# Optimization experiments

Hardware: AMD Instinct MI355X
Metric: run time of the kernel (lower is better)

## Reference

```python
import jax, jax.numpy as jnp
import numpy as np

L = 64       # num_steps
NHID = 256   # nhid
N = 64       # cache_N
TOPK = 8     # cache_k


def setup_inputs() -> dict:
    key = jax.random.key(0)
    k1, k2, k3 = jax.random.split(key, 3)
    query = jax.random.normal(k1, (1, L, 32, NHID), dtype=jnp.float32)
    keys = jax.random.normal(k2, (N, 32, L * NHID), dtype=jnp.float32)       # stacked key_i buffers
    values = jax.random.normal(k3, (N, L, 32, 4 * NHID), dtype=jnp.float32)  # stacked value_i buffers, (nlayers+1)*nhid=1024
    return {"query": query, "keys": keys, "values": values}


def reference(query, keys, values):
    # query: (query_len=1, L, bsz, nhid) -> transpose(1,2) -> (1, bsz, L, nhid)
    q = jnp.swapaxes(query, 1, 2)
    qlen, bsz = q.shape[0], q.shape[1]
    q = q.reshape(qlen, bsz, -1)                 # no_summary: (1, bsz, dk)
    keys_t = jnp.swapaxes(keys, 0, 1)            # (bsz, N, dk)
    _vals = jnp.einsum('klbh->bklh', values)     # (bsz, N, L, h); computed in original, unused in max_pooling branch
    # max_pooling branch
    q2 = q.reshape(-1, L, NHID)                  # (bsz, L, nhid)
    pk = keys_t.reshape(-1, N, L, NHID)          # (bsz, N, L, nhid)
    att = jnp.einsum('bih,bnjh->bijn', q2, pk)   # (bsz, L, L, N)
    att = att.reshape(-1, L * L, 1, N).max(axis=1)  # (bsz, 1, N) max-pool over all step pairs
    att = att.reshape(-1, 1, N)
    _, topk_idx = jax.lax.top_k(att, TOPK)       # (bsz, 1, topk)
    topk_idx = jnp.squeeze(topk_idx, axis=1).T   # (topk, bsz)
    return att, topk_idx
```

## Files before the change

kernel.cpp:

```cpp
#include <hip/hip_runtime.h>
#include <hip/hip_bf16.h>
#include <math.h>

namespace {

constexpr int L   = 64;
constexpr int NH  = 256;
constexpr int NC  = 64;
constexpr int BSZ = 32;

typedef float f32x16 __attribute__((ext_vector_type(16)));
typedef short bf16x8 __attribute__((ext_vector_type(8)));

__device__ inline void split8(const float4 x0, const float4 x1,
                              bf16x8& hi, bf16x8& lo) {
  float f[8];
  *(float4*)(f)     = x0;
  *(float4*)(f + 4) = x1;
#pragma unroll
  for (int q = 0; q < 8; ++q) {
    const __hip_bfloat16 h = __float2bfloat16(f[q]);
    unsigned short hu;
    __builtin_memcpy(&hu, &h, 2);
    const float hf = __builtin_bit_cast(float, (unsigned)hu << 16);
    const __hip_bfloat16 l = __float2bfloat16(f[q] - hf);
    unsigned short lu;
    __builtin_memcpy(&lu, &l, 2);
    hi[q] = (short)hu;
    lo[q] = (short)lu;
  }
}

__global__ __launch_bounds__(256, 2) void attmax_mfma(
    const float* __restrict__ query,
    const float* __restrict__ keys,
    float* __restrict__ out)
{
  __shared__ __align__(16) short Qhi[2 * 16 * 64 * 8];
  __shared__ __align__(16) short Qlo[2 * 16 * 64 * 8];

  const unsigned X = blockIdx.x;
  const int b = ((X >> 7) << 3) | (X & 7);
  const int g = (X >> 3) & 15;

  const int tid  = threadIdx.x;
  const int w    = tid >> 6;
  const int lane = tid & 63;
  const int r    = lane & 31;
  const int h    = lane >> 5;

  for (int s = tid; s < 2048; s += 256) {
    const int it = s >> 10;
    const int kc = (s >> 6) & 15;
    const int sl = s & 63;
    const int row = it * 32 + (sl & 31);
    const int kof = kc * 16 + (sl >> 5) * 8;
    const float* src = query + ((size_t)row * BSZ + b) * NH + kof;
    bf16x8 hi, lo;
    split8(*(const float4*)src, *(const float4*)(src + 4), hi, lo);
    *(bf16x8*)&Qhi[s * 8] = hi;
    *(bf16x8*)&Qlo[s * 8] = lo;
  }
  __syncthreads();

  const int n = g * 4 + w;
  const float* kb = keys + ((size_t)n * BSZ + b) * (size_t)(L * NH);
  const float* kp = kb + (size_t)r * NH + h * 8;

  f32x16 acc[2][2];
#pragma unroll
  for (int i = 0; i < 2; ++i)
#pragma unroll
    for (int j = 0; j < 2; ++j)
#pragma unroll
      for (int e = 0; e < 16; ++e) acc[i][j][e] = 0.f;

  float4 bufA[4], bufB[4];

#define LOAD_K(buf, kc)                                                  \
  do {                                                                   \
    const float* p0 = kp + (kc) * 16;                                    \
    (buf)[0] = *(const float4*)(p0);                                     \
    (buf)[1] = *(const float4*)(p0 + 4);                                 \
    const float* p1 = p0 + 32 * NH;                                      \
    (buf)[2] = *(const float4*)(p1);                                     \
    (buf)[3] = *(const float4*)(p1 + 4);                                 \
  } while (0)

#define COMPUTE(buf, kc)                                                 \
  do {                                                                   \
    bf16x8 bh0, bl0, bh1, bl1;                                           \
    split8((buf)[0], (buf)[1], bh0, bl0);                                \
    split8((buf)[2], (buf)[3], bh1, bl1);                                \
    bf16x8 ah[2], al[2];                                                 \
    _Pragma("unroll")                                                    \
    for (int it = 0; it < 2; ++it) {                                     \
      const int slot = ((it * 16 + (kc)) * 64 + lane) * 8;               \
      ah[it] = *(const bf16x8*)&Qhi[slot];                               \
      al[it] = *(const bf16x8*)&Qlo[slot];                               \
    }                                                                    \
    _Pragma("unroll")                                                    \
    for (int it = 0; it < 2; ++it) {                                     \
      acc[it][0] = __builtin_amdgcn_mfma_f32_32x32x16_bf16(al[it], bh0, acc[it][0], 0, 0, 0); \
      acc[it][0] = __builtin_amdgcn_mfma_f32_32x32x16_bf16(ah[it], bl0, acc[it][0], 0, 0, 0); \
      acc[it][0] = __builtin_amdgcn_mfma_f32_32x32x16_bf16(ah[it], bh0, acc[it][0], 0, 0, 0); \
      acc[it][1] = __builtin_amdgcn_mfma_f32_32x32x16_bf16(al[it], bh1, acc[it][1], 0, 0, 0); \
      acc[it][1] = __builtin_amdgcn_mfma_f32_32x32x16_bf16(ah[it], bl1, acc[it][1], 0, 0, 0); \
      acc[it][1] = __builtin_amdgcn_mfma_f32_32x32x16_bf16(ah[it], bh1, acc[it][1], 0, 0, 0); \
    }                                                                    \
  } while (0)

  LOAD_K(bufA, 0);
#pragma unroll
  for (int kc = 0; kc < 16; kc += 2) {
    if (kc + 1 < 16) LOAD_K(bufB, kc + 1);
    COMPUTE(bufA, kc);
    if (kc + 2 < 16) LOAD_K(bufA, kc + 2);
    COMPUTE(bufB, kc + 1);
  }
#undef LOAD_K
#undef COMPUTE

  float m = -INFINITY;
#pragma unroll
  for (int i = 0; i < 2; ++i)
#pragma unroll
    for (int j = 0; j < 2; ++j)
#pragma unroll
      for (int e = 0; e < 16; ++e) m = fmaxf(m, acc[i][j][e]);

#pragma unroll
  for (int off = 1; off < 64; off <<= 1)
    m = fmaxf(m, __shfl_xor(m, off, 64));

  if (lane == 0) out[(size_t)b * NC + n] = m;
}

__global__ __launch_bounds__(64) void topk_kernel(float* __restrict__ out) {
  const int b = blockIdx.x;
  const int l = threadIdx.x;
  float v = out[b * NC + l];
#pragma unroll
  for (int k = 0; k < 8; ++k) {
    float bv = v;
    int bi = l;
#pragma unroll
    for (int off = 1; off < 64; off <<= 1) {
      const float ov = __shfl_xor(bv, off, 64);
      const int oi = __shfl_xor(bi, off, 64);
      if (ov > bv || (ov == bv && oi < bi)) { bv = ov; bi = oi; }
    }
    if (l == 0) out[BSZ * NC + k * BSZ + b] = (float)bi;
    if (l == bi) v = -INFINITY;
  }
}

}

extern "C" void kernel_launch(void* const* d_in, const int* in_sizes, int n_in,
                              void* d_out, int out_size, void* d_ws, size_t ws_size,
                              hipStream_t stream) {
  const float* query = (const float*)d_in[0];
  const float* keys  = (const float*)d_in[1];
  float* out = (float*)d_out;

  attmax_mfma<<<dim3(512), dim3(256), 0, stream>>>(query, keys, out);
  topk_kernel<<<dim3(BSZ), dim3(64), 0, stream>>>(out);
}
```

Measured before the change: 38.99 us.

## Precompute split query once per batch and double waves per key

The bf16 hi/lo split of the query moves into a separate kernel that writes it to workspace once per batch element. The main kernel then copies that data into LDS with global_load_lds. The main kernel now runs 512 threads per block, with two waves per key vector, each handling half of the key rows. This cuts per-wave register use and raises parallelism for the memory-bound key stream. The two waves' partial maxima are combined through shared memory. The cost is one extra kernel launch, a workspace round trip, and a 64KB LDS footprint per block. That footprint may limit residency below the requested 4 blocks per CU.

```diff
diff --git a/kernel.cpp b/kernel.cpp
--- a/kernel.cpp
+++ b/kernel.cpp
@@ -31,25 +31,20 @@
   }
 }
 
-__global__ __launch_bounds__(256, 2) void attmax_mfma(
-    const float* __restrict__ query,
-    const float* __restrict__ keys,
-    float* __restrict__ out)
-{
-  __shared__ __align__(16) short Qhi[2 * 16 * 64 * 8];
-  __shared__ __align__(16) short Qlo[2 * 16 * 64 * 8];
+__device__ inline void gl16(const void* g, void* l) {
+  __builtin_amdgcn_global_load_lds(
+      (const __attribute__((address_space(1))) unsigned*)(g),
+      (__attribute__((address_space(3))) unsigned*)(l), 16, 0, 0);
+}
 
-  const unsigned X = blockIdx.x;
-  const int b = ((X >> 7) << 3) | (X & 7);
-  const int g = (X >> 3) & 15;
-
-  const int tid  = threadIdx.x;
-  const int w    = tid >> 6;
-  const int lane = tid & 63;
-  const int r    = lane & 31;
-  const int h    = lane >> 5;
-
-  for (int s = tid; s < 2048; s += 256) {
+__global__ __launch_bounds__(256) void qsplit_kernel(
+    const float* __restrict__ query, char* __restrict__ ws) {
+  const int b   = blockIdx.x;
+  const int tid = threadIdx.x;
+  char* wb = ws + (size_t)b * 65536;
+#pragma unroll
+  for (int rr = 0; rr < 8; ++rr) {
+    const int s  = tid + rr * 256;
     const int it = s >> 10;
     const int kc = (s >> 6) & 15;
     const int sl = s & 63;
@@ -58,56 +53,72 @@
     const float* src = query + ((size_t)row * BSZ + b) * NH + kof;
     bf16x8 hi, lo;
     split8(*(const float4*)src, *(const float4*)(src + 4), hi, lo);
-    *(bf16x8*)&Qhi[s * 8] = hi;
-    *(bf16x8*)&Qlo[s * 8] = lo;
+    *(bf16x8*)(wb + (size_t)s * 16)         = hi;
+    *(bf16x8*)(wb + 32768 + (size_t)s * 16) = lo;
+  }
+}
+
+__global__ __launch_bounds__(512, 4) void attmax_mfma(
+    const float* __restrict__ keys,
+    const char* __restrict__ ws,
+    float* __restrict__ out)
+{
+  __shared__ __align__(16) char qlds[64 * 1024];
+  __shared__ float wm[8];
+  const short* Qhi = (const short*)qlds;
+  const short* Qlo = (const short*)(qlds + 32768);
+
+  const unsigned X = blockIdx.x;
+  const int b  = X & 31;
+  const int ng = X >> 5;
+
+  const int tid  = threadIdx.x;
+  const int w    = tid >> 6;
+  const int lane = tid & 63;
+  const int n    = ng * 4 + (w >> 1);
+  const int jt   = w & 1;
+
+  {
+    const char* src = ws + (size_t)b * 65536;
+#pragma unroll
+    for (int q = 0; q < 8; ++q) {
+      const int off = (q * 8 + w) * 1024;
+      gl16(src + off + lane * 16, qlds + off);
+    }
   }
   __syncthreads();
 
-  const int n = g * 4 + w;
-  const float* kb = keys + ((size_t)n * BSZ + b) * (size_t)(L * NH);
-  const float* kp = kb + (size_t)r * NH + h * 8;
+  const float* kp = keys + ((size_t)n * BSZ + b) * (size_t)(L * NH)
+                  + (size_t)(jt * 32 + (lane & 31)) * NH + (lane >> 5) * 8;
 
-  f32x16 acc[2][2];
+  f32x16 acc[2];
 #pragma unroll
-  for (int i = 0; i < 2; ++i)
+  for (int it = 0; it < 2; ++it)
 #pragma unroll
-    for (int j = 0; j < 2; ++j)
-#pragma unroll
-      for (int e = 0; e < 16; ++e) acc[i][j][e] = 0.f;
+    for (int e = 0; e < 16; ++e) acc[it][e] = 0.f;
 
-  float4 bufA[4], bufB[4];
+  float4 bufA[2], bufB[2];
 
-#define LOAD_K(buf, kc)                                                  \
-  do {                                                                   \
-    const float* p0 = kp + (kc) * 16;                                    \
-    (buf)[0] = *(const float4*)(p0);                                     \
-    (buf)[1] = *(const float4*)(p0 + 4);                                 \
-    const float* p1 = p0 + 32 * NH;                                      \
-    (buf)[2] = *(const float4*)(p1);                                     \
-    (buf)[3] = *(const float4*)(p1 + 4);                                 \
+#define LOAD_K(buf, kc)                                  \
+  do {                                                   \
+    const float* p0 = kp + (kc) * 16;                    \
+    (buf)[0] = *(const float4*)(p0);                     \
+    (buf)[1] = *(const float4*)(p0 + 4);                 \
   } while (0)
 
-#define COMPUTE(buf, kc)                                                 \
-  do {                                                                   \
-    bf16x8 bh0, bl0, bh1, bl1;                                           \
-    split8((buf)[0], (buf)[1], bh0, bl0);                                \
-    split8((buf)[2], (buf)[3], bh1, bl1);                                \
-    bf16x8 ah[2], al[2];                                                 \
-    _Pragma("unroll")                                                    \
-    for (int it = 0; it < 2; ++it) {                                     \
-      const int slot = ((it * 16 + (kc)) * 64 + lane) * 8;               \
-      ah[it] = *(const bf16x8*)&Qhi[slot];                               \
-      al[it] = *(const bf16x8*)&Qlo[slot];                               \
-    }                                                                    \
-    _Pragma("unroll")                                                    \
-    for (int it = 0; it < 2; ++it) {                                     \
-      acc[it][0] = __builtin_amdgcn_mfma_f32_32x32x16_bf16(al[it], bh0, acc[it][0], 0, 0, 0); \
-      acc[it][0] = __builtin_amdgcn_mfma_f32_32x32x16_bf16(ah[it], bl0, acc[it][0], 0, 0, 0); \
-      acc[it][0] = __builtin_amdgcn_mfma_f32_32x32x16_bf16(ah[it], bh0, acc[it][0], 0, 0, 0); \
-      acc[it][1] = __builtin_amdgcn_mfma_f32_32x32x16_bf16(al[it], bh1, acc[it][1], 0, 0, 0); \
-      acc[it][1] = __builtin_amdgcn_mfma_f32_32x32x16_bf16(ah[it], bl1, acc[it][1], 0, 0, 0); \
-      acc[it][1] = __builtin_amdgcn_mfma_f32_32x32x16_bf16(ah[it], bh1, acc[it][1], 0, 0, 0); \
-    }                                                                    \
+#define COMPUTE(buf, kc)                                                      \
+  do {                                                                        \
+    bf16x8 bh, bl;                                                            \
+    split8((buf)[0], (buf)[1], bh, bl);                                       \
+    _Pragma("unroll")                                                         \
+    for (int it = 0; it < 2; ++it) {                                          \
+      const int slot = ((it * 16 + (kc)) * 64 + lane) * 8;                    \
+      const bf16x8 ah = *(const bf16x8*)&Qhi[slot];                           \
+      const bf16x8 al = *(const bf16x8*)&Qlo[slot];                           \
+      acc[it] = __builtin_amdgcn_mfma_f32_32x32x16_bf16(al, bh, acc[it], 0, 0, 0); \
+      acc[it] = __builtin_amdgcn_mfma_f32_32x32x16_bf16(ah, bl, acc[it], 0, 0, 0); \
+      acc[it] = __builtin_amdgcn_mfma_f32_32x32x16_bf16(ah, bh, acc[it], 0, 0, 0); \
+    }                                                                         \
   } while (0)
 
   LOAD_K(bufA, 0);
@@ -123,17 +134,17 @@
 
   float m = -INFINITY;
 #pragma unroll
-  for (int i = 0; i < 2; ++i)
+  for (int it = 0; it < 2; ++it)
 #pragma unroll
-    for (int j = 0; j < 2; ++j)
-#pragma unroll
-      for (int e = 0; e < 16; ++e) m = fmaxf(m, acc[i][j][e]);
-
+    for (int e = 0; e < 16; ++e) m = fmaxf(m, acc[it][e]);
 #pragma unroll
   for (int off = 1; off < 64; off <<= 1)
     m = fmaxf(m, __shfl_xor(m, off, 64));
 
-  if (lane == 0) out[(size_t)b * NC + n] = m;
+  if (lane == 0) wm[w] = m;
+  __syncthreads();
+  if (lane == 0 && (w & 1) == 0)
+    out[(size_t)b * NC + n] = fmaxf(wm[w], wm[w + 1]);
 }
 
 __global__ __launch_bounds__(64) void topk_kernel(float* __restrict__ out) {
@@ -163,7 +174,9 @@
   const float* query = (const float*)d_in[0];
   const float* keys  = (const float*)d_in[1];
   float* out = (float*)d_out;
+  char*  ws  = (char*)d_ws;
 
-  attmax_mfma<<<dim3(512), dim3(256), 0, stream>>>(query, keys, out);
+  qsplit_kernel<<<dim3(BSZ), dim3(256), 0, stream>>>(query, ws);
+  attmax_mfma<<<dim3(512), dim3(512), 0, stream>>>(keys, ws, out);
   topk_kernel<<<dim3(BSZ), dim3(64), 0, stream>>>(out);
 }
```

Result: slower. 40.30 us (+3.3%).
